# Performance work log

Hardware: AMD Instinct MI355X
Metric: run time of the kernel (lower is better)

The kernel has to match this reference:

```python
import jax, jax.numpy as jnp
import numpy as np

N, P1, P2, D = 4, 8192, 8192, 3
BIG = 1e10  # masks out padded target points before top-k (pytorch3d uses +inf)


def setup_inputs() -> dict:
    key = jax.random.key(0)
    k1, k2, k3 = jax.random.split(key, 3)
    pred_points = jax.random.normal(k1, (N, P1, D), dtype=jnp.float32)
    target_points = jax.random.normal(k2, (N, P2, D), dtype=jnp.float32)
    # ragged target lengths in [P2//2, P2] (always > 0 so every batch element is 'visible')
    target_lengths = jax.random.randint(k3, (N,), P2 // 2, P2 + 1, dtype=jnp.int32)
    return {
        "pred_points": pred_points,
        "target_points": target_points,
        "target_lengths": target_lengths,
        "num_neighbours": 1,
    }


def reference(pred_points, target_points, target_lengths, num_neighbours):
    x, y = pred_points, target_points  # [N,P1,D], [N,P2,D]
    n, p1, _ = x.shape
    p2 = y.shape[1]
    x2 = jnp.sum(x * x, axis=-1)
    y2 = jnp.sum(y * y, axis=-1)
    d2 = x2[:, :, None] + y2[:, None, :] - 2.0 * jnp.einsum('nid,njd->nij', x, y)
    d2 = jnp.maximum(d2, 0.0)

    # mask of invalid (padded) target points per batch: j >= target_lengths[b]
    y_pad = jnp.arange(p2)[None, :] >= target_lengths[:, None]  # [N,P2]

    # knn_points(x -> y): invalid y columns pushed to BIG before top-k smallest
    dxy = jnp.where(y_pad[:, None, :], BIG, d2)
    nn_x = -jax.lax.top_k(-dxy, num_neighbours)[0]          # [N,P1,K]
    cham_x = jnp.sum(jnp.mean(nn_x, axis=-1), axis=1) / p1  # point_reduction='mean'

    # knn_points(y -> x): all x points valid; zero out padded y rows afterwards
    dyx = jnp.swapaxes(d2, 1, 2)                            # [N,P2,P1]
    nn_y = -jax.lax.top_k(-dyx, num_neighbours)[0]          # [N,P2,K]
    cham_y_pts = jnp.where(y_pad, 0.0, jnp.mean(nn_y, axis=-1))
    cham_y = jnp.sum(cham_y_pts, axis=1) / target_lengths.astype(x.dtype)

    # batch_reduction='mean'
    loss = (jnp.sum(cham_x) + jnp.sum(cham_y)) / n
    return loss
```

## Files before the change

kernel.cpp:

```cpp
#include <hip/hip_runtime.h>

constexpr int N = 4;
constexpr int P = 8192;
constexpr int TILE = 256;
constexpr int MI = 4;
constexpr int CHUNKS = 8;
constexpr int RT = 32;
constexpr int ROWS = RT * MI;
constexpr int BLK_PER_B = P / ROWS;

__global__ __launch_bounds__(256) void chamfer_fused_kernel(
    const float* __restrict__ pred, const float* __restrict__ targ,
    const int* __restrict__ lens, float* __restrict__ out)
{
    const bool xtoy = (blockIdx.z == 0);
    const int b    = blockIdx.x / BLK_PER_B;
    const int rt   = blockIdx.x % BLK_PER_B;
    const int row0 = rt * ROWS;
    const int L    = lens[b];
    const int tid  = threadIdx.x;
    const int chunk   = tid >> 5;
    const int rowtile = tid & 31;

    if (!xtoy && row0 >= L) return;

    const float* rows = xtoy ? pred : targ;
    const float* cols = xtoy ? targ : pred;
    const float* rbase = rows + (size_t)b * P * 3;
    const float* cbase = cols + (size_t)b * P * 3;

    __shared__ float4 sy[TILE];
    __shared__ float  sx2[ROWS];
    __shared__ float  red[ROWS * CHUNKS];
    __shared__ float  acc[4];

    float rx[MI], ry[MI], rz[MI], best[MI];
    #pragma unroll
    for (int k = 0; k < MI; ++k) {
        const int r = rowtile * MI + k;
        const float* p = rbase + (size_t)(row0 + r) * 3;
        rx[k] = p[0]; ry[k] = p[1]; rz[k] = p[2];
        best[k] = 1e30f;
        if (chunk == 0)
            sx2[r] = rx[k]*rx[k] + ry[k]*ry[k] + rz[k]*rz[k];
    }

    const int ntiles = xtoy ? (L + TILE - 1) / TILE : P / TILE;

    for (int t = 0; t < ntiles; ++t) {
        const int col = t * TILE + tid;
        float4 cv;
        if (xtoy && col >= L) {
            cv = make_float4(0.f, 0.f, 0.f, 1e30f);
        } else {
            const float* p = cbase + (size_t)col * 3;
            const float a = p[0], bb = p[1], cc = p[2];
            cv = make_float4(-2.f*a, -2.f*bb, -2.f*cc, a*a + bb*bb + cc*cc);
        }
        __syncthreads();
        sy[tid] = cv;
        __syncthreads();

        const float4* sp = &sy[chunk * 32];
        #pragma unroll 8
        for (int jj = 0; jj < 32; ++jj) {
            const float4 q = sp[jj];
            #pragma unroll
            for (int k = 0; k < MI; ++k) {
                float d = fmaf(rz[k], q.z, q.w);
                d = fmaf(ry[k], q.y, d);
                d = fmaf(rx[k], q.x, d);
                best[k] = fminf(best[k], d);
            }
        }
    }

    #pragma unroll
    for (int k = 0; k < MI; ++k)
        red[(rowtile * MI + k) * CHUNKS + chunk] = best[k];
    __syncthreads();

    float c = 0.f;
    if (tid < ROWS) {
        float v = red[tid * CHUNKS];
        #pragma unroll
        for (int i = 1; i < CHUNKS; ++i) v = fminf(v, red[tid * CHUNKS + i]);
        const float d2 = fmaxf(v + sx2[tid], 0.f);
        if (xtoy)                 c = d2 * (1.0f / ((float)P * (float)N));
        else if (row0 + tid < L)  c = d2 / ((float)L * (float)N);
    }
    #pragma unroll
    for (int off = 32; off; off >>= 1) c += __shfl_down(c, off, 64);
    if ((tid & 63) == 0) acc[tid >> 6] = c;
    __syncthreads();
    if (tid == 0) atomicAdd(out, acc[0] + acc[1] + acc[2] + acc[3]);
}

extern "C" void kernel_launch(void* const* d_in, const int* in_sizes, int n_in,
                              void* d_out, int out_size, void* d_ws, size_t ws_size,
                              hipStream_t stream)
{
    const float* pred = (const float*)d_in[0];
    const float* targ = (const float*)d_in[1];
    const int*   lens = (const int*)d_in[2];
    float* out = (float*)d_out;

    hipMemsetAsync(out, 0, out_size * sizeof(float), stream);
    dim3 grid(N * BLK_PER_B, 1, 2);
    chamfer_fused_kernel<<<grid, 256, 0, stream>>>(pred, targ, lens, out);
}
```

Measured before the change: 111.4 us.

## Split column range into segments with larger row tiles and a separate reduce pass

Each block now handles 512 rows (16 per thread) against one of eight column segments rather than all columns, writing partial minima to workspace. A second kernel takes the min across segments, applies clamping and scaling, and accumulates the loss. This raises register-level reuse of each shared-memory column load and keeps enough blocks in flight for load balance. The cost is workspace traffic, an extra launch, and higher register pressure with the 4-blocks-per-CU launch bound.

```diff
diff --git a/kernel.cpp b/kernel.cpp
--- a/kernel.cpp
+++ b/kernel.cpp
@@ -2,55 +2,59 @@
 
 constexpr int N = 4;
 constexpr int P = 8192;
+constexpr int NSEG = 8;
+constexpr int SEGC = P / NSEG;
 constexpr int TILE = 256;
-constexpr int MI = 4;
-constexpr int CHUNKS = 8;
-constexpr int RT = 32;
-constexpr int ROWS = RT * MI;
-constexpr int BLK_PER_B = P / ROWS;
+constexpr int ROWS = 512;
+constexpr int MI = 16;
+constexpr int RGROUPS = P / ROWS;
 
-__global__ __launch_bounds__(256) void chamfer_fused_kernel(
+__global__ __launch_bounds__(256, 4) void chamfer_min_kernel(
     const float* __restrict__ pred, const float* __restrict__ targ,
-    const int* __restrict__ lens, float* __restrict__ out)
+    const int* __restrict__ lens, float* __restrict__ ws)
 {
-    const bool xtoy = (blockIdx.z == 0);
-    const int b    = blockIdx.x / BLK_PER_B;
-    const int rt   = blockIdx.x % BLK_PER_B;
-    const int row0 = rt * ROWS;
+    int id = blockIdx.x;
+    const int seg = id & (NSEG - 1);    id /= NSEG;
+    const int rg  = id & (RGROUPS - 1); id /= RGROUPS;
+    const int b   = id & (N - 1);       id /= N;
+    const int dir = id;
+    const int row0 = rg * ROWS;
+    const int c0   = seg * SEGC;
     const int L    = lens[b];
     const int tid  = threadIdx.x;
     const int chunk   = tid >> 5;
     const int rowtile = tid & 31;
 
-    if (!xtoy && row0 >= L) return;
+    float* slot = ws + (((size_t)dir * N + b) * NSEG + seg) * P + row0;
 
-    const float* rows = xtoy ? pred : targ;
-    const float* cols = xtoy ? targ : pred;
-    const float* rbase = rows + (size_t)b * P * 3;
-    const float* cbase = cols + (size_t)b * P * 3;
+    if (dir == 1 && row0 >= L) return;
+    if (dir == 0 && c0 >= L) {
+        reinterpret_cast<float2*>(slot)[tid] = make_float2(1e30f, 1e30f);
+        return;
+    }
 
-    __shared__ float4 sy[TILE];
-    __shared__ float  sx2[ROWS];
-    __shared__ float  red[ROWS * CHUNKS];
-    __shared__ float  acc[4];
+    const float* rbase = (dir == 0 ? pred : targ) + (size_t)b * P * 3;
+    const float* cbase = (dir == 0 ? targ : pred) + (size_t)b * P * 3;
 
     float rx[MI], ry[MI], rz[MI], best[MI];
     #pragma unroll
     for (int k = 0; k < MI; ++k) {
-        const int r = rowtile * MI + k;
-        const float* p = rbase + (size_t)(row0 + r) * 3;
+        const float* p = rbase + (size_t)(row0 + rowtile + 32 * k) * 3;
         rx[k] = p[0]; ry[k] = p[1]; rz[k] = p[2];
         best[k] = 1e30f;
-        if (chunk == 0)
-            sx2[r] = rx[k]*rx[k] + ry[k]*ry[k] + rz[k]*rz[k];
     }
 
-    const int ntiles = xtoy ? (L + TILE - 1) / TILE : P / TILE;
+    __shared__ float4 sy[TILE];
+    __shared__ float  red[ROWS * 9];
 
-    for (int t = 0; t < ntiles; ++t) {
-        const int col = t * TILE + tid;
+    int vc = SEGC;
+    if (dir == 0 && L - c0 < SEGC) vc = L - c0;
+    const int nt = (vc + TILE - 1) / TILE;
+
+    for (int t = 0; t < nt; ++t) {
+        const int col = c0 + t * TILE + tid;
         float4 cv;
-        if (xtoy && col >= L) {
+        if (dir == 0 && col >= L) {
             cv = make_float4(0.f, 0.f, 0.f, 1e30f);
         } else {
             const float* p = cbase + (size_t)col * 3;
@@ -62,38 +66,66 @@
         __syncthreads();
 
         const float4* sp = &sy[chunk * 32];
-        #pragma unroll 8
-        for (int jj = 0; jj < 32; ++jj) {
-            const float4 q = sp[jj];
+        #pragma unroll 2
+        for (int jj = 0; jj < 32; jj += 2) {
+            const float4 q0 = sp[jj];
+            const float4 q1 = sp[jj + 1];
             #pragma unroll
             for (int k = 0; k < MI; ++k) {
-                float d = fmaf(rz[k], q.z, q.w);
-                d = fmaf(ry[k], q.y, d);
-                d = fmaf(rx[k], q.x, d);
-                best[k] = fminf(best[k], d);
+                float d0 = fmaf(rx[k], q0.x, fmaf(ry[k], q0.y, fmaf(rz[k], q0.z, q0.w)));
+                float d1 = fmaf(rx[k], q1.x, fmaf(ry[k], q1.y, fmaf(rz[k], q1.z, q1.w)));
+                best[k] = fminf(best[k], fminf(d0, d1));
             }
         }
     }
 
     #pragma unroll
     for (int k = 0; k < MI; ++k)
-        red[(rowtile * MI + k) * CHUNKS + chunk] = best[k];
+        red[(rowtile + 32 * k) * 9 + chunk] = best[k];
+    if (chunk == 0) {
+        #pragma unroll
+        for (int k = 0; k < MI; ++k)
+            red[(rowtile + 32 * k) * 9 + 8] =
+                fmaf(rx[k], rx[k], fmaf(ry[k], ry[k], rz[k] * rz[k]));
+    }
     __syncthreads();
 
+    {
+        const float* r0 = &red[(tid * 2) * 9];
+        const float* r1 = &red[(tid * 2 + 1) * 9];
+        float v0 = fminf(fminf(fminf(r0[0], r0[1]), fminf(r0[2], r0[3])),
+                         fminf(fminf(r0[4], r0[5]), fminf(r0[6], r0[7]))) + r0[8];
+        float v1 = fminf(fminf(fminf(r1[0], r1[1]), fminf(r1[2], r1[3])),
+                         fminf(fminf(r1[4], r1[5]), fminf(r1[6], r1[7]))) + r1[8];
+        reinterpret_cast<float2*>(slot)[tid] = make_float2(v0, v1);
+    }
+}
+
+__global__ __launch_bounds__(256) void chamfer_reduce_kernel(
+    const float* __restrict__ ws, const int* __restrict__ lens,
+    float* __restrict__ out)
+{
+    const int item = blockIdx.x * 256 + threadIdx.x;
+    const int dir = item >> 15;
+    const int b   = (item >> 13) & (N - 1);
+    const int p   = item & (P - 1);
+    const int L   = lens[b];
+
     float c = 0.f;
-    if (tid < ROWS) {
-        float v = red[tid * CHUNKS];
+    if (dir == 0 || p < L) {
+        const float* base = ws + (((size_t)dir * N + b) * NSEG) * P + p;
+        float v = base[0];
         #pragma unroll
-        for (int i = 1; i < CHUNKS; ++i) v = fminf(v, red[tid * CHUNKS + i]);
-        const float d2 = fmaxf(v + sx2[tid], 0.f);
-        if (xtoy)                 c = d2 * (1.0f / ((float)P * (float)N));
-        else if (row0 + tid < L)  c = d2 / ((float)L * (float)N);
+        for (int s = 1; s < NSEG; ++s) v = fminf(v, base[(size_t)s * P]);
+        v = fmaxf(v, 0.f);
+        c = dir ? v / ((float)L * (float)N) : v * (1.0f / ((float)P * (float)N));
     }
     #pragma unroll
     for (int off = 32; off; off >>= 1) c += __shfl_down(c, off, 64);
-    if ((tid & 63) == 0) acc[tid >> 6] = c;
+    __shared__ float acc[4];
+    if ((threadIdx.x & 63) == 0) acc[threadIdx.x >> 6] = c;
     __syncthreads();
-    if (tid == 0) atomicAdd(out, acc[0] + acc[1] + acc[2] + acc[3]);
+    if (threadIdx.x == 0) atomicAdd(out, acc[0] + acc[1] + acc[2] + acc[3]);
 }
 
 extern "C" void kernel_launch(void* const* d_in, const int* in_sizes, int n_in,
@@ -104,8 +136,10 @@
     const float* targ = (const float*)d_in[1];
     const int*   lens = (const int*)d_in[2];
     float* out = (float*)d_out;
+    float* ws  = (float*)d_ws;
 
     hipMemsetAsync(out, 0, out_size * sizeof(float), stream);
-    dim3 grid(N * BLK_PER_B, 1, 2);
-    chamfer_fused_kernel<<<grid, 256, 0, stream>>>(pred, targ, lens, out);
+    const int nblk = 2 * N * RGROUPS * NSEG;
+    chamfer_min_kernel<<<nblk, 256, 0, stream>>>(pred, targ, lens, ws);
+    chamfer_reduce_kernel<<<(2 * N * P) / 256, 256, 0, stream>>>(ws, lens, out);
 }
```

After: 107.6 us. -3.4%, faster.
